# Optimization experiments

Hardware: AMD Instinct MI355X
Metric: run time of the kernel (lower is better)

## Reference

```python
import jax, jax.numpy as jnp
import numpy as np

B, T, D, H = 16, 2048, 1024, 512  # input_size D == 2*H (bidirectional, k=3 highway)


def setup_inputs() -> dict:
    key = jax.random.key(0)
    k1, k2 = jax.random.split(key, 2)
    x = jax.random.normal(k1, (B, T, D), dtype=jnp.float32)
    # W: [D, dir, H, 3] -> slices: 0 = x_tilde, 1 = f-gate preact, 2 = r-gate preact
    W = jax.random.normal(k2, (D, 2, H, 3), dtype=jnp.float32) / np.sqrt(D)
    # bias: [dir, 2, H] -> bias[:,0]=b_f, bias[:,1]=b_r
    bias = jnp.zeros((2, 2, H), dtype=jnp.float32)
    return {"x": x, "W": W, "bias": bias}


def _scan_dir(g0, f, r, xres):
    """Elementwise SRU recurrence over time. All inputs [T, B, H]."""
    def step(c, inp):
        g_t, f_t, r_t, x_t = inp
        c = f_t * c + (1.0 - f_t) * g_t
        h = r_t * jnp.tanh(c) + (1.0 - r_t) * x_t
        return c, h
    c_last, h = jax.lax.scan(step, jnp.zeros_like(g0[0]), (g0, f, r, xres))
    return h, c_last  # [T,B,H], [B,H]


def _sru(x, W, bias):
    xt = jnp.swapaxes(x, 0, 1)                      # [T, B, D]
    U = jnp.einsum('tbd,dzhk->tbzhk', xt, W)        # [T, B, dir, H, 3]
    g0 = U[..., 0]                                  # [T, B, 2, H]
    f = jax.nn.sigmoid(U[..., 1] + bias[:, 0])      # broadcast [2,H]
    r = jax.nn.sigmoid(U[..., 2] + bias[:, 1])
    xres = xt.reshape(T, B, 2, H)                   # highway residual per direction (k=3)

    # forward direction
    h_f, c_f = _scan_dir(g0[:, :, 0], f[:, :, 0], r[:, :, 0], xres[:, :, 0])
    # backward direction: flip time, scan, flip back
    h_b, c_b = _scan_dir(g0[::-1, :, 1], f[::-1, :, 1], r[::-1, :, 1], xres[::-1, :, 1])
    h_b = h_b[::-1]

    out = jnp.concatenate([h_f, h_b], axis=-1)      # [T, B, 2H]
    c_last = jnp.concatenate([c_f, c_b], axis=-1)   # [B, 2H]
    return out, c_last


def reference(x, W, bias):
    out, c_last = _sru(x, W, bias)
    # wrapper transposes back to batch-first; c: (layers=1, B, 2H) -> (B, 1, 2H)
    return jnp.swapaxes(out, 0, 1), c_last[:, None, :]
```

## Files before the change

### kernel.cpp

```cpp
#include <hip/hip_runtime.h>
#include <cstdint>

typedef unsigned int uint;
typedef unsigned short ushort;
typedef __attribute__((ext_vector_type(8))) __bf16 bf16x8;
typedef __attribute__((ext_vector_type(4))) float f32x4;
typedef __attribute__((ext_vector_type(4))) ushort us4;

#define BB 16
#define TT 2048
#define DD 1024
#define HH 512

__device__ inline ushort f2bf(float f) {
    uint u = __float_as_uint(f);
    u += 0x7FFF + ((u >> 16) & 1);
    return (ushort)(u >> 16);
}
__device__ inline float bf2f(ushort b) {
    return __uint_as_float(((uint)b) << 16);
}
__device__ inline float sigm(float x) { return 1.f / (1.f + __expf(-x)); }
__device__ inline float4 ld4(const float* p) { return *(const float4*)p; }

__device__ inline void gload16(const void* g, void* l) {
    __builtin_amdgcn_global_load_lds(
        (const __attribute__((address_space(1))) uint*)g,
        (__attribute__((address_space(3))) uint*)l, 16, 0, 0);
}

__global__ __launch_bounds__(256) void convert_W(const float* __restrict__ W,
                                                 ushort* __restrict__ Bth,
                                                 ushort* __restrict__ Btl) {
    int idx = blockIdx.x * 256 + threadIdx.x;
    int d   = idx & 1023;
    int n   = idx >> 10;
    int z    = n / 1536;
    int rem  = n % 1536;
    int gate = rem >> 9;
    int h    = rem & 511;
    float w    = W[(size_t)d * 3072 + z * 1536 + h * 3 + gate];
    ushort whi = f2bf(w);
    Bth[idx]   = whi;
    Btl[idx]   = f2bf(w - bf2f(whi));
}

__global__ __launch_bounds__(256, 2) void gemm_bf16split(
    const float* __restrict__ x, const ushort* __restrict__ Bth,
    const ushort* __restrict__ Btl, float* __restrict__ C) {
    __shared__ ushort lds[4 * 128 * 32];

    const int t    = threadIdx.x;
    const int w    = t >> 6;
    const int lane = t & 63;
    const size_t m0 = (size_t)blockIdx.x * 128;
    const size_t n0 = (size_t)blockIdx.y * 128;
    const int wm = w >> 1, wn = w & 1;

    f32x4 acc[4][4];
#pragma unroll
    for (int i = 0; i < 4; i++)
#pragma unroll
        for (int j = 0; j < 4; j++) acc[i][j] = (f32x4)(0.f);

    const int srow  = w * 32 + (lane >> 2);
    const int kphys = lane & 3;
    const int frow  = lane & 15;
    const int fkoff = (((lane >> 4) ^ ((frow >> 1) & 3)) << 3);

    float4 xv[4];
#pragma unroll
    for (int p = 0; p < 4; p++) {
        int ridx = p * 256 + t;
        int row  = ridx >> 3;
        int kq   = ridx & 7;
        xv[p] = ld4(x + (m0 + row) * 1024 + kq * 4);
    }

    for (int k0 = 0; k0 < 1024; k0 += 32) {
#pragma unroll
        for (int arr = 0; arr < 2; arr++) {
            const ushort* G = arr ? Btl : Bth;
#pragma unroll
            for (int c = 0; c < 2; c++) {
                const int row = srow + c * 16;
                const int kcl = kphys ^ ((row >> 1) & 3);
                const ushort* src = G + ((n0 + row) << 10) + k0 + (kcl << 3);
                char* dst = (char*)lds + (2 + arr) * 8192 +
                            (w * 32 + c * 16) * 64 + lane * 16;
                gload16(src, dst);
            }
        }
#pragma unroll
        for (int p = 0; p < 4; p++) {
            int ridx = p * 256 + t;
            int row  = ridx >> 3;
            int kq   = ridx & 7;
            int off  = row * 64 + (((kq >> 1) ^ ((row >> 1) & 3)) << 4) +
                       ((kq & 1) << 3);
            float vf[4] = {xv[p].x, xv[p].y, xv[p].z, xv[p].w};
            us4 hi, lo;
#pragma unroll
            for (int j = 0; j < 4; j++) {
                ushort h = f2bf(vf[j]);
                hi[j]    = h;
                lo[j]    = f2bf(vf[j] - bf2f(h));
            }
            *(us4*)((char*)lds + off)        = hi;
            *(us4*)((char*)lds + 8192 + off) = lo;
        }
        __syncthreads();

        bf16x8 fa[4], fal[4], fb[4], fbl[4];
#pragma unroll
        for (int i = 0; i < 4; i++) {
            const int ra = (wm * 64 + i * 16 + frow) * 32;
            const int rb = (wn * 64 + i * 16 + frow) * 32;
            fa[i]  = *(const bf16x8*)&lds[0 * 4096 + ra + fkoff];
            fal[i] = *(const bf16x8*)&lds[1 * 4096 + ra + fkoff];
            fb[i]  = *(const bf16x8*)&lds[2 * 4096 + rb + fkoff];
            fbl[i] = *(const bf16x8*)&lds[3 * 4096 + rb + fkoff];
        }

        const int k0n = (k0 + 32) & 1023;
        float4 xn[4];
#pragma unroll
        for (int p = 0; p < 4; p++) {
            int ridx = p * 256 + t;
            int row  = ridx >> 3;
            int kq   = ridx & 7;
            xn[p] = ld4(x + (m0 + row) * 1024 + k0n + kq * 4);
        }

#pragma unroll
        for (int i = 0; i < 4; i++)
#pragma unroll
            for (int j = 0; j < 4; j++) {
                acc[i][j] = __builtin_amdgcn_mfma_f32_16x16x32_bf16(
                    fa[i], fb[j], acc[i][j], 0, 0, 0);
                acc[i][j] = __builtin_amdgcn_mfma_f32_16x16x32_bf16(
                    fa[i], fbl[j], acc[i][j], 0, 0, 0);
                acc[i][j] = __builtin_amdgcn_mfma_f32_16x16x32_bf16(
                    fal[i], fb[j], acc[i][j], 0, 0, 0);
            }
        __syncthreads();
#pragma unroll
        for (int p = 0; p < 4; p++) xv[p] = xn[p];
    }

    const int ccol = lane & 15;
    const int crow = (lane >> 4) * 4;
#pragma unroll
    for (int i = 0; i < 4; i++) {
        const size_t mrow = m0 + wm * 64 + i * 16 + crow;
#pragma unroll
        for (int j = 0; j < 4; j++) {
            const size_t ncol = n0 + wn * 64 + j * 16 + ccol;
            float* Cp = C + mrow * 3072 + ncol;
#pragma unroll
            for (int r = 0; r < 4; r++) Cp[(size_t)r * 3072] = acc[i][j][r];
        }
    }
}

#define SCH 16384
#define NCH 32
#define CL 64

#define STEPA(CC, FA, G, FP, BF)          \
    {                                     \
        float ff = sigm((FP) + (BF));     \
        CC = ff * CC + (1.f - ff) * (G);  \
        FA *= ff;                         \
    }

#define STEPC(CC, G, FP, RP, XV, BF, BR, OUT)       \
    {                                               \
        float ff = sigm((FP) + (BF));               \
        float rr = sigm((RP) + (BR));               \
        CC = ff * CC + (1.f - ff) * (G);            \
        float e  = __expf(2.f * CC);                \
        float th = 1.f - 2.f / (e + 1.f);           \
        OUT = rr * th + (1.f - rr) * (XV);          \
    }

__global__ __launch_bounds__(256) void scanA(const float* __restrict__ U,
                                             const float* __restrict__ bias,
                                             float* __restrict__ F,
                                             float* __restrict__ Cp) {
    int tid = blockIdx.x * 256 + threadIdx.x;
    int s   = tid >> 12;
    int ci  = tid & 4095;
    int b = ci >> 8, z = (ci >> 7) & 1, h4 = (ci & 127) << 2;
    float4 bf = ld4(&bias[z * 1024 + h4]);
    const float* Ub = U + (size_t)b * TT * 3072 + z * 1536 + h4;
    float4 c  = {0.f, 0.f, 0.f, 0.f};
    float4 Fa = {1.f, 1.f, 1.f, 1.f};
#pragma unroll 4
    for (int q = 0; q < CL; q++) {
        int n = s * CL + q;
        int t = z ? (TT - 1 - n) : n;
        size_t o = (size_t)t * 3072;
        float4 g = ld4(Ub + o);
        float4 f = ld4(Ub + o + 512);
        STEPA(c.x, Fa.x, g.x, f.x, bf.x);
        STEPA(c.y, Fa.y, g.y, f.y, bf.y);
        STEPA(c.z, Fa.z, g.z, f.z, bf.z);
        STEPA(c.w, Fa.w, g.w, f.w, bf.w);
    }
    *(float4*)&F[((size_t)s << 14) + (ci << 2)]  = Fa;
    *(float4*)&Cp[((size_t)s << 14) + (ci << 2)] = c;
}

__global__ __launch_bounds__(256) void scanB(const float* __restrict__ F,
                                             const float* __restrict__ Cp,
                                             float* __restrict__ cstart) {
    int ci = blockIdx.x * 256 + threadIdx.x;
    float4 c = {0.f, 0.f, 0.f, 0.f};
    for (int s = 0; s < NCH; s++) {
        size_t o = ((size_t)s << 14) + (ci << 2);
        *(float4*)&cstart[o] = c;
        float4 Fv = ld4(&F[o]);
        float4 Cv = ld4(&Cp[o]);
        c.x = Fv.x * c.x + Cv.x;
        c.y = Fv.y * c.y + Cv.y;
        c.z = Fv.z * c.z + Cv.z;
        c.w = Fv.w * c.w + Cv.w;
    }
}

__global__ __launch_bounds__(256) void scanC(const float* __restrict__ U,
                                             const float* __restrict__ x,
                                             const float* __restrict__ bias,
                                             const float* __restrict__ cstart,
                                             float* __restrict__ out) {
    int tid = blockIdx.x * 256 + threadIdx.x;
    int s   = tid >> 12;
    int ci  = tid & 4095;
    int b = ci >> 8, z = (ci >> 7) & 1, h4 = (ci & 127) << 2;
    float4 bf = ld4(&bias[z * 1024 + h4]);
    float4 br = ld4(&bias[z * 1024 + 512 + h4]);
    const float* Ub = U + (size_t)b * TT * 3072 + z * 1536 + h4;
    const float* xb = x + (size_t)b * TT * 1024 + z * 512 + h4;
    float* ob       = out + (size_t)b * TT * 1024 + z * 512 + h4;
    float4 c = ld4(&cstart[((size_t)s << 14) + (ci << 2)]);
#pragma unroll 2
    for (int q = 0; q < CL; q++) {
        int n = s * CL + q;
        int t = z ? (TT - 1 - n) : n;
        size_t o = (size_t)t * 3072;
        float4 g  = ld4(Ub + o);
        float4 f  = ld4(Ub + o + 512);
        float4 r  = ld4(Ub + o + 1024);
        float4 xv = ld4(xb + (size_t)t * 1024);
        float4 hv;
        STEPC(c.x, g.x, f.x, r.x, xv.x, bf.x, br.x, hv.x);
        STEPC(c.y, g.y, f.y, r.y, xv.y, bf.y, br.y, hv.y);
        STEPC(c.z, g.z, f.z, r.z, xv.z, bf.z, br.z, hv.z);
        STEPC(c.w, g.w, f.w, r.w, xv.w, bf.w, br.w, hv.w);
        *(float4*)(ob + (size_t)t * 1024) = hv;
    }
    if (s == NCH - 1)
        *(float4*)(out + (size_t)BB * TT * 1024 + b * 1024 + z * 512 + h4) = c;
}

extern "C" void kernel_launch(void* const* d_in, const int* in_sizes, int n_in,
                              void* d_out, int out_size, void* d_ws,
                              size_t ws_size, hipStream_t stream) {
    const float* x    = (const float*)d_in[0];
    const float* W    = (const float*)d_in[1];
    const float* bias = (const float*)d_in[2];
    float* out        = (float*)d_out;

    char* ws    = (char*)d_ws;
    float* U    = (float*)ws;
    ushort* Bth = (ushort*)(ws + 402653184UL);
    ushort* Btl = (ushort*)(ws + 408944640UL);
    float* F    = (float*)(ws + 402653184UL);
    float* Cp   = (float*)(ws + 404750336UL);
    float* cst  = (float*)(ws + 406847488UL);

    convert_W<<<12288, 256, 0, stream>>>(W, Bth, Btl);

    dim3 grid(256, 24);
    gemm_bf16split<<<grid, 256, 0, stream>>>(x, Bth, Btl, U);

    scanA<<<512, 256, 0, stream>>>(U, bias, F, Cp);
    scanB<<<16, 256, 0, stream>>>(F, Cp, cst);
    scanC<<<512, 256, 0, stream>>>(U, x, bias, cst, out);
}
```

Before: 1.017 ms.

## Tile W conversion through LDS, drop x prefetch, double scan chunk count

convert_W now loads W tiles into shared memory with coalesced float4 reads and writes the hi/lo bf16 split with vectorized stores, replacing strided scalar gathers. The GEMM no longer prefetches the next x slice into registers and loads the current slice at the top of each iteration, which lowers register pressure but exposes global load latency. The scan is split into 64 chunks of 32 steps instead of 32 of 64, with scanA and scanC launched on twice as many blocks and workspace offsets moved to fit the larger buffers. This raises parallelism in the chunked scan at the cost of more work in the sequential scanB stage.

Result: no change. 1.007 ms (-1.1%).

```diff
diff --git a/kernel.cpp b/kernel.cpp
--- a/kernel.cpp
+++ b/kernel.cpp
@@ -32,17 +32,46 @@
 __global__ __launch_bounds__(256) void convert_W(const float* __restrict__ W,
                                                  ushort* __restrict__ Bth,
                                                  ushort* __restrict__ Btl) {
-    int idx = blockIdx.x * 256 + threadIdx.x;
-    int d   = idx & 1023;
-    int n   = idx >> 10;
-    int z    = n / 1536;
-    int rem  = n % 1536;
-    int gate = rem >> 9;
-    int h    = rem & 511;
-    float w    = W[(size_t)d * 3072 + z * 1536 + h * 3 + gate];
-    ushort whi = f2bf(w);
-    Bth[idx]   = whi;
-    Btl[idx]   = f2bf(w - bf2f(whi));
+    __shared__ float tile[64][193];
+    const int bid = blockIdx.x;
+    const int d0  = (bid >> 4) * 64;
+    const int z   = (bid >> 3) & 1;
+    const int h0  = (bid & 7) * 64;
+
+    const float* Wb = W + z * 1536 + h0 * 3;
+#pragma unroll
+    for (int i = 0; i < 12; i++) {
+        int f   = i * 256 + threadIdx.x;
+        int row = f / 48;
+        int c4  = f % 48;
+        float4 v = ld4(Wb + (size_t)(d0 + row) * 3072 + c4 * 4);
+        tile[row][c4 * 4 + 0] = v.x;
+        tile[row][c4 * 4 + 1] = v.y;
+        tile[row][c4 * 4 + 2] = v.z;
+        tile[row][c4 * 4 + 3] = v.w;
+    }
+    __syncthreads();
+
+    const int dd4 = (threadIdx.x & 15) * 4;
+#pragma unroll
+    for (int g = 0; g < 3; g++) {
+#pragma unroll
+        for (int j = 0; j < 4; j++) {
+            int nn = (threadIdx.x >> 4) + j * 16;
+            us4 hi, lo;
+#pragma unroll
+            for (int i = 0; i < 4; i++) {
+                float wv = tile[dd4 + i][nn * 3 + g];
+                ushort h = f2bf(wv);
+                hi[i]    = h;
+                lo[i]    = f2bf(wv - bf2f(h));
+            }
+            size_t n   = (size_t)z * 1536 + g * 512 + h0 + nn;
+            size_t off = (n << 10) + d0 + dd4;
+            *(us4*)(Bth + off) = hi;
+            *(us4*)(Btl + off) = lo;
+        }
+    }
 }
 
 __global__ __launch_bounds__(256, 2) void gemm_bf16split(
@@ -68,16 +97,15 @@
     const int frow  = lane & 15;
     const int fkoff = (((lane >> 4) ^ ((frow >> 1) & 3)) << 3);
 
-    float4 xv[4];
-#pragma unroll
-    for (int p = 0; p < 4; p++) {
-        int ridx = p * 256 + t;
-        int row  = ridx >> 3;
-        int kq   = ridx & 7;
-        xv[p] = ld4(x + (m0 + row) * 1024 + kq * 4);
-    }
-
     for (int k0 = 0; k0 < 1024; k0 += 32) {
+        float4 xv[4];
+#pragma unroll
+        for (int p = 0; p < 4; p++) {
+            int ridx = p * 256 + t;
+            int row  = ridx >> 3;
+            int kq   = ridx & 7;
+            xv[p] = ld4(x + (m0 + row) * 1024 + k0 + kq * 4);
+        }
 #pragma unroll
         for (int arr = 0; arr < 2; arr++) {
             const ushort* G = arr ? Btl : Bth;
@@ -121,17 +149,6 @@
             fb[i]  = *(const bf16x8*)&lds[2 * 4096 + rb + fkoff];
             fbl[i] = *(const bf16x8*)&lds[3 * 4096 + rb + fkoff];
         }
-
-        const int k0n = (k0 + 32) & 1023;
-        float4 xn[4];
-#pragma unroll
-        for (int p = 0; p < 4; p++) {
-            int ridx = p * 256 + t;
-            int row  = ridx >> 3;
-            int kq   = ridx & 7;
-            xn[p] = ld4(x + (m0 + row) * 1024 + k0n + kq * 4);
-        }
-
 #pragma unroll
         for (int i = 0; i < 4; i++)
 #pragma unroll
@@ -144,8 +161,6 @@
                     fal[i], fb[j], acc[i][j], 0, 0, 0);
             }
         __syncthreads();
-#pragma unroll
-        for (int p = 0; p < 4; p++) xv[p] = xn[p];
     }
 
     const int ccol = lane & 15;
@@ -164,8 +179,8 @@
 }
 
 #define SCH 16384
-#define NCH 32
-#define CL 64
+#define NCH 64
+#define CL 32
 
 #define STEPA(CC, FA, G, FP, BF)          \
     {                                     \
@@ -277,15 +292,15 @@
     ushort* Bth = (ushort*)(ws + 402653184UL);
     ushort* Btl = (ushort*)(ws + 408944640UL);
     float* F    = (float*)(ws + 402653184UL);
-    float* Cp   = (float*)(ws + 404750336UL);
-    float* cst  = (float*)(ws + 406847488UL);
-
-    convert_W<<<12288, 256, 0, stream>>>(W, Bth, Btl);
+    float* Cp   = (float*)(ws + 406847488UL);
+    float* cst  = (float*)(ws + 411041792UL);
+
+    convert_W<<<256, 256, 0, stream>>>(W, Bth, Btl);
 
     dim3 grid(256, 24);
     gemm_bf16split<<<grid, 256, 0, stream>>>(x, Bth, Btl, U);
 
-    scanA<<<512, 256, 0, stream>>>(U, bias, F, Cp);
+    scanA<<<1024, 256, 0, stream>>>(U, bias, F, Cp);
     scanB<<<16, 256, 0, stream>>>(F, Cp, cst);
-    scanC<<<512, 256, 0, stream>>>(U, x, bias, cst, out);
-}
+    scanC<<<1024, 256, 0, stream>>>(U, x, bias, cst, out);
+}
```
